# Performance work log

Hardware: AMD Instinct MI355X
Metric: run time of the kernel (lower is better)

Reference implementation:

```python
import jax, jax.numpy as jnp
import numpy as np

B, T, IN, H, OUT = 4096, 7, 512, 1024, 512


def setup_inputs() -> dict:
    key = jax.random.key(0)
    ks = jax.random.split(key, 13)
    s = 0.05  # weight init scale to keep gates/tanh unsaturated
    return {
        "x": jax.random.normal(ks[0], (B, T, IN), jnp.float32),
        "W_ih1": jax.random.normal(ks[1], (3 * H, IN), jnp.float32) * s,
        "W_hh1": jax.random.normal(ks[2], (3 * H, H), jnp.float32) * s,
        "b_ih1": jax.random.normal(ks[3], (3 * H,), jnp.float32) * s,
        "b_hh1": jax.random.normal(ks[4], (3 * H,), jnp.float32) * s,
        "W_ih2": jax.random.normal(ks[5], (3 * H, H), jnp.float32) * s,
        "W_hh2": jax.random.normal(ks[6], (3 * H, H), jnp.float32) * s,
        "b_ih2": jax.random.normal(ks[7], (3 * H,), jnp.float32) * s,
        "b_hh2": jax.random.normal(ks[8], (3 * H,), jnp.float32) * s,
        "Wo1": jax.random.normal(ks[9], (OUT, H), jnp.float32) * s,
        "bo1": jax.random.normal(ks[10], (OUT,), jnp.float32) * s,
        "Wo2": jax.random.normal(ks[11], (OUT, H), jnp.float32) * s,
        "bo2": jax.random.normal(ks[12], (OUT,), jnp.float32) * s,
    }


def gru_cell(x, h, W_ih, W_hh, b_ih, b_hh):
    # torch.nn.GRUCell math, gate order (r, z, n)
    gi = x @ W_ih.T + b_ih          # [B, 3H]
    gh = h @ W_hh.T + b_hh          # [B, 3H]
    i_r, i_z, i_n = jnp.split(gi, 3, axis=-1)
    h_r, h_z, h_n = jnp.split(gh, 3, axis=-1)
    r = jax.nn.sigmoid(i_r + h_r)
    z = jax.nn.sigmoid(i_z + h_z)
    n = jnp.tanh(i_n + r * h_n)
    return (1.0 - z) * n + z * h


def reference(x, W_ih1, W_hh1, b_ih1, b_hh1, W_ih2, W_hh2, b_ih2, b_hh2,
              Wo1, bo1, Wo2, bo2):
    batch = x.shape[0]
    h1_0 = jnp.zeros((batch, H), x.dtype)
    h2_0 = jnp.zeros((batch, H), x.dtype)

    def step(carry, x_t):
        h1, h2 = carry
        h1 = gru_cell(x_t, h1, W_ih1, W_hh1, b_ih1, b_hh1)
        h2 = gru_cell(h1, h2, W_ih2, W_hh2, b_ih2, b_hh2)
        out = jnp.tanh(h1 @ Wo1.T + bo1) + jnp.tanh(h2 @ Wo2.T + bo2)
        # s_t_cached starts as T zeros and only T steps run, so the popped
        # cached state is always zeros: mse(h2, 0) == mean(h2**2)
        aux = jnp.mean(jnp.square(h2))
        return (h1, h2), (out, aux)

    xs = jnp.swapaxes(x, 0, 1)  # [T, B, IN]
    _, (outs, auxs) = jax.lax.scan(step, (h1_0, h2_0), xs)
    outputs = jnp.swapaxes(outs, 0, 1)  # [B, T, OUT]
    aux_loss = jnp.sum(auxs)
    return outputs, aux_loss
```

## Files before the change

### kernel.cpp

```cpp
#include <hip/hip_runtime.h>
#include <cstdint>

#define BB   4096
#define TT   7
#define INF  512
#define HH   1024
#define OUTF 512
#define G3   3072

typedef short bf16x8 __attribute__((ext_vector_type(8)));
typedef float f32x4  __attribute__((ext_vector_type(4)));

static __device__ __forceinline__ unsigned short f2bf(float f) {
  unsigned u = __float_as_uint(f);
  unsigned r = ((u >> 16) & 1u) + 0x7FFFu;
  return (unsigned short)((u + r) >> 16);
}
static __device__ __forceinline__ float bf2f(unsigned short s) {
  return __uint_as_float(((unsigned)s) << 16);
}

#define GLDS16(gp, lp)                                                        \
  __builtin_amdgcn_global_load_lds(                                           \
      (const __attribute__((address_space(1))) void*)(gp),                    \
      (__attribute__((address_space(3))) void*)(lp), 16, 0, 0)

__device__ __forceinline__ int xcd_swz(int bid, int nwg) {
  return (bid & 7) * (nwg >> 3) + (bid >> 3);
}

__global__ __launch_bounds__(256)
void cvt_f32_to_bf16_x4(const float* __restrict__ in, unsigned short* __restrict__ out, int n4) {
  int i = blockIdx.x * 256 + threadIdx.x;
  if (i >= n4) return;
  const float4 v = ((const float4*)in)[i];
  ushort4 o;
  o.x = f2bf(v.x); o.y = f2bf(v.y); o.z = f2bf(v.z); o.w = f2bf(v.w);
  ((ushort4*)out)[i] = o;
}

template<int BM, int BN, int WM, int WN, int GN>
__device__ __forceinline__ void gemm_core(
    const unsigned short* __restrict__ A, long lda, long bm,
    const unsigned short* __restrict__ Wp, long ldw, int K,
    const float* __restrict__ biasp,
    void* __restrict__ Cp, long ldc,
    const float* __restrict__ addp, long ldadd, int mode)
{
  constexpr int AR = (BM * 8) / 256;
  constexpr int WR = (BN * 8) / 256;
  __shared__ __attribute__((aligned(16))) unsigned short sm[(BM + BN) * 64];
  unsigned short* As = sm;
  unsigned short* Ws = sm + BM * 64;
  __attribute__((address_space(3))) unsigned short* lAs =
      (__attribute__((address_space(3))) unsigned short*)As;
  __attribute__((address_space(3))) unsigned short* lWs =
      (__attribute__((address_space(3))) unsigned short*)Ws;

  const int tid  = threadIdx.x;
  const int lane = tid & 63;
  const int wid  = tid >> 6;
  const int wr = (wid / GN) * (WM * 16);
  const int wc = (wid % GN) * (WN * 16);
  const int fr = lane & 15;
  const int q2 = lane >> 4;

  const unsigned short* gpa[AR];
  const unsigned short* gpw[WR];
  int lofa[AR], lofw[WR];
#pragma unroll
  for (int r = 0; r < AR; ++r) {
    const int id = r * 256 + tid;
    const int row = id >> 3, cc = id & 7;
    gpa[r] = A + (bm + row) * lda + (cc ^ (row & 7)) * 8;
    lofa[r] = id * 8;
  }
#pragma unroll
  for (int r = 0; r < WR; ++r) {
    const int id = r * 256 + tid;
    const int row = id >> 3, cc = id & 7;
    gpw[r] = Wp + (long)row * ldw + (cc ^ (row & 7)) * 8;
    lofw[r] = id * 8;
  }

  f32x4 acc[WM][WN] = {};
  for (int kt = 0; kt < K; kt += 64) {
    if (kt) __syncthreads();
#pragma unroll
    for (int r = 0; r < AR; ++r) GLDS16(gpa[r] + kt, lAs + lofa[r]);
#pragma unroll
    for (int r = 0; r < WR; ++r) GLDS16(gpw[r] + kt, lWs + lofw[r]);
    __syncthreads();

#pragma unroll
    for (int ks = 0; ks < 2; ++ks) {
      bf16x8 af[WM], wf[WN];
#pragma unroll
      for (int i = 0; i < WM; ++i) {
        const int row = wr + i * 16 + fr;
        const int ch  = (ks * 4 + q2) ^ (row & 7);
        af[i] = *(const bf16x8*)&As[row * 64 + ch * 8];
      }
#pragma unroll
      for (int i = 0; i < WN; ++i) {
        const int row = wc + i * 16 + fr;
        const int ch  = (ks * 4 + q2) ^ (row & 7);
        wf[i] = *(const bf16x8*)&Ws[row * 64 + ch * 8];
      }
#pragma unroll
      for (int mi = 0; mi < WM; ++mi)
#pragma unroll
        for (int ni = 0; ni < WN; ++ni)
          acc[mi][ni] = __builtin_amdgcn_mfma_f32_16x16x32_bf16(af[mi], wf[ni], acc[mi][ni], 0, 0, 0);
    }
  }

  const int q = lane >> 4;
#pragma unroll
  for (int ni = 0; ni < WN; ++ni) {
    const int col = wc + ni * 16 + fr;
    const float bv = biasp[col];
#pragma unroll
    for (int mi = 0; mi < WM; ++mi) {
      const long row = bm + wr + mi * 16 + q * 4;
#pragma unroll
      for (int j = 0; j < 4; ++j) {
        const float v = acc[mi][ni][j] + bv;
        if (mode == 0)      ((float*)Cp)[(row + j) * ldc + col] = v;
        else if (mode == 1) ((float*)Cp)[(row + j) * ldc + col] = tanhf(v);
        else if (mode == 2) ((float*)Cp)[(row + j) * ldc + col] = tanhf(v) + addp[(row + j) * ldadd + col];
        else                ((unsigned short*)Cp)[(row + j) * ldc + col] = f2bf(v);
      }
    }
  }
}

__global__ __launch_bounds__(256)
void k_gi1(const unsigned short* __restrict__ A, long lda,
           const unsigned short* __restrict__ W, const float* __restrict__ bias,
           unsigned short* __restrict__ C, int gx)
{
  const int wg = xcd_swz(blockIdx.x, gridDim.x);
  const int bx = wg % gx, by = wg / gx;
  gemm_core<128,128,4,4,2>(A, lda, (long)bx * 128, W + (long)by * 128 * INF, INF, INF,
                           bias + by * 128, C + by * 128, G3, nullptr, 0, 3);
}

__global__ __launch_bounds__(256)
void k_gh_dual(const unsigned short* __restrict__ h1b, const unsigned short* __restrict__ h2b,
               const unsigned short* __restrict__ W1, const unsigned short* __restrict__ W2,
               const float* __restrict__ b1, const float* __restrict__ b2,
               float* __restrict__ gh1, float* __restrict__ gh2)
{
  const int wg = xcd_swz(blockIdx.x, gridDim.x);
  const int bx = wg % 32;
  const int by = (wg / 32) % 24;
  const int z  = wg / (32 * 24);
  const unsigned short* Aa = z ? h2b : h1b;
  const unsigned short* Ww = (z ? W2 : W1) + (long)by * 128 * HH;
  const float* bias = (z ? b2 : b1) + by * 128;
  float* C = (z ? gh2 : gh1) + by * 128;
  gemm_core<128,128,4,4,2>(Aa, HH, (long)bx * 128, Ww, HH, HH, bias, C, G3, nullptr, 0, 0);
}

__global__ __launch_bounds__(256)
void k_gi2_o1(const unsigned short* __restrict__ h1b,
              const unsigned short* __restrict__ Wih2, const float* __restrict__ bih2,
              float* __restrict__ gi2,
              const unsigned short* __restrict__ Wo1, const float* __restrict__ bo1,
              float* __restrict__ o1t)
{
  const int wg = xcd_swz(blockIdx.x, gridDim.x);
  const int bx = wg % 32;
  const int by = wg / 32;
  const bool g = (by < 24);
  const int bo = by - 24;
  const unsigned short* Ww = g ? (Wih2 + (long)by * 128 * HH) : (Wo1 + (long)bo * 128 * HH);
  const float* bias        = g ? (bih2 + by * 128)            : (bo1 + bo * 128);
  void* C                  = g ? (void*)(gi2 + by * 128)      : (void*)(o1t + bo * 128);
  const long ldc           = g ? (long)G3 : (long)OUTF;
  gemm_core<128,128,4,4,2>(h1b, HH, (long)bx * 128, Ww, HH, HH, bias, C, ldc,
                           nullptr, 0, g ? 0 : 1);
}

__global__ __launch_bounds__(256)
void k_o2_out(const unsigned short* __restrict__ h2b,
              const unsigned short* __restrict__ Wo2, const float* __restrict__ bo2,
              const float* __restrict__ o1t, float* __restrict__ outp)
{
  const int wg = xcd_swz(blockIdx.x, gridDim.x);
  const int bx = wg % 64;
  const int by = wg / 64;
  gemm_core<64,64,2,2,2>(h2b, HH, (long)bx * 64, Wo2 + (long)by * 64 * HH, HH, HH,
                         bo2 + by * 64, outp + by * 64, (long)TT * OUTF,
                         o1t + by * 64, OUTF, 2);
}

template<bool GIBF>
__global__ __launch_bounds__(256)
void k_gate(const void* __restrict__ gi, long gistride,
            const float* __restrict__ gh,
            unsigned short* __restrict__ hb,
            float* __restrict__ auxp)
{
  const int i4 = blockIdx.x * 256 + threadIdx.x;
  const int e  = i4 << 2;
  const int b = e >> 10;
  const int c = e & 1023;
  f32x4 ir, iz, inn;
  if (GIBF) {
    const unsigned short* g = (const unsigned short*)gi + (long)b * gistride + c;
    const ushort4 a0 = *(const ushort4*)(g);
    const ushort4 a1 = *(const ushort4*)(g + HH);
    const ushort4 a2 = *(const ushort4*)(g + 2 * HH);
    ir  = f32x4{bf2f(a0.x), bf2f(a0.y), bf2f(a0.z), bf2f(a0.w)};
    iz  = f32x4{bf2f(a1.x), bf2f(a1.y), bf2f(a1.z), bf2f(a1.w)};
    inn = f32x4{bf2f(a2.x), bf2f(a2.y), bf2f(a2.z), bf2f(a2.w)};
  } else {
    const float* g = (const float*)gi + (long)b * gistride + c;
    ir = *(const f32x4*)g; iz = *(const f32x4*)(g + HH); inn = *(const f32x4*)(g + 2 * HH);
  }
  const float* ghp = gh + (long)b * G3 + c;
  const f32x4 hr = *(const f32x4*)ghp;
  const f32x4 hz = *(const f32x4*)(ghp + HH);
  const f32x4 hn = *(const f32x4*)(ghp + 2 * HH);
  const ushort4 ho = *(const ushort4*)(hb + e);
  const f32x4 h = f32x4{bf2f(ho.x), bf2f(ho.y), bf2f(ho.z), bf2f(ho.w)};
  f32x4 hnew;
  float vsum = 0.f;
#pragma unroll
  for (int j = 0; j < 4; ++j) {
    const float r = 1.f / (1.f + __expf(-(ir[j] + hr[j])));
    const float z = 1.f / (1.f + __expf(-(iz[j] + hz[j])));
    const float n = tanhf(inn[j] + r * hn[j]);
    hnew[j] = (1.f - z) * n + z * h[j];
    vsum += hnew[j] * hnew[j];
  }
  ushort4 o;
  o.x = f2bf(hnew[0]); o.y = f2bf(hnew[1]); o.z = f2bf(hnew[2]); o.w = f2bf(hnew[3]);
  *(ushort4*)(hb + e) = o;
  if (auxp != nullptr) {
#pragma unroll
    for (int off = 32; off > 0; off >>= 1) vsum += __shfl_down(vsum, off);
    __shared__ float wsum[4];
    if ((threadIdx.x & 63) == 0) wsum[threadIdx.x >> 6] = vsum;
    __syncthreads();
    if (threadIdx.x == 0) auxp[blockIdx.x] = wsum[0] + wsum[1] + wsum[2] + wsum[3];
  }
}

__global__ __launch_bounds__(256)
void aux_reduce(const float* __restrict__ p, int n, float* __restrict__ out, float scale) {
  float s = 0.f;
  for (int i = threadIdx.x; i < n; i += 256) s += p[i];
#pragma unroll
  for (int off = 32; off > 0; off >>= 1) s += __shfl_down(s, off);
  __shared__ float wsum[4];
  if ((threadIdx.x & 63) == 0) wsum[threadIdx.x >> 6] = s;
  __syncthreads();
  if (threadIdx.x == 0) out[0] = (wsum[0] + wsum[1] + wsum[2] + wsum[3]) * scale;
}

extern "C" void kernel_launch(void* const* d_in, const int* in_sizes, int n_in,
                              void* d_out, int out_size, void* d_ws, size_t ws_size,
                              hipStream_t stream) {
  const float* x    = (const float*)d_in[0];
  const float* Wih1 = (const float*)d_in[1];
  const float* Whh1 = (const float*)d_in[2];
  const float* bih1 = (const float*)d_in[3];
  const float* bhh1 = (const float*)d_in[4];
  const float* Wih2 = (const float*)d_in[5];
  const float* Whh2 = (const float*)d_in[6];
  const float* bih2 = (const float*)d_in[7];
  const float* bhh2 = (const float*)d_in[8];
  const float* Wo1  = (const float*)d_in[9];
  const float* bo1  = (const float*)d_in[10];
  const float* Wo2  = (const float*)d_in[11];
  const float* bo2  = (const float*)d_in[12];

  char* ws = (char*)d_ws;
  size_t off = 0;
  auto alloc = [&](size_t bytes) {
    char* p = ws + off;
    off = (off + bytes + 255) & ~(size_t)255;
    return p;
  };

  unsigned short* xb    = (unsigned short*)alloc((size_t)BB * TT * INF * 2);
  unsigned short* wih1b = (unsigned short*)alloc((size_t)G3 * INF * 2);
  unsigned short* whh1b = (unsigned short*)alloc((size_t)G3 * HH * 2);
  unsigned short* wih2b = (unsigned short*)alloc((size_t)G3 * HH * 2);
  unsigned short* whh2b = (unsigned short*)alloc((size_t)G3 * HH * 2);
  unsigned short* wo1b  = (unsigned short*)alloc((size_t)OUTF * HH * 2);
  unsigned short* wo2b  = (unsigned short*)alloc((size_t)OUTF * HH * 2);
  unsigned short* h1b = (unsigned short*)alloc((size_t)BB * HH * 2);
  unsigned short* h2b = (unsigned short*)alloc((size_t)BB * HH * 2);
  float* gh1  = (float*)alloc((size_t)BB * G3 * 4);
  float* gh2  = (float*)alloc((size_t)BB * G3 * 4);
  float* o1t  = (float*)alloc((size_t)BB * OUTF * 4);
  float* auxp = (float*)alloc((size_t)TT * (BB * HH / 1024) * 4);
  float* gi2  = gh1;

  const size_t gi1_big   = (size_t)BB * TT * G3 * 2;
  const size_t gi1_small = (size_t)BB * G3 * 2;
  const bool hoist = (off + gi1_big + (size_t)(32 << 20)) <= ws_size;
  unsigned short* gi1b = (unsigned short*)alloc(hoist ? gi1_big : gi1_small);

  float* aux = (float*)d_out + (size_t)BB * TT * OUTF;

  auto cvt = [&](const float* src, unsigned short* dst, size_t n) {
    int n4 = (int)(n / 4);
    cvt_f32_to_bf16_x4<<<dim3((n4 + 255) / 256), dim3(256), 0, stream>>>(src, dst, n4);
  };
  cvt(x,    xb,    (size_t)BB * TT * INF);
  cvt(Wih1, wih1b, (size_t)G3 * INF);
  cvt(Whh1, whh1b, (size_t)G3 * HH);
  cvt(Wih2, wih2b, (size_t)G3 * HH);
  cvt(Whh2, whh2b, (size_t)G3 * HH);
  cvt(Wo1,  wo1b,  (size_t)OUTF * HH);
  cvt(Wo2,  wo2b,  (size_t)OUTF * HH);

  hipMemsetAsync(h1b, 0, (size_t)BB * HH * 2, stream);
  hipMemsetAsync(h2b, 0, (size_t)BB * HH * 2, stream);

  const dim3 blk(256);
  const int gateGrid = BB * HH / 1024;

  if (hoist)
    k_gi1<<<dim3(224 * 24), blk, 0, stream>>>(xb, INF, wih1b, bih1, gi1b, 224);

  for (int t = 0; t < TT; ++t) {
    if (!hoist)
      k_gi1<<<dim3(32 * 24), blk, 0, stream>>>(xb + (size_t)t * INF, (long)TT * INF,
                                               wih1b, bih1, gi1b, 32);
    k_gh_dual<<<dim3(32 * 24 * 2), blk, 0, stream>>>(h1b, h2b, whh1b, whh2b, bhh1, bhh2, gh1, gh2);
    k_gate<true><<<dim3(gateGrid), blk, 0, stream>>>(
        hoist ? gi1b + (size_t)t * G3 : gi1b, hoist ? (long)TT * G3 : (long)G3,
        gh1, h1b, nullptr);
    k_gi2_o1<<<dim3(32 * 28), blk, 0, stream>>>(h1b, wih2b, bih2, gi2, wo1b, bo1, o1t);
    k_gate<false><<<dim3(gateGrid), blk, 0, stream>>>(gi2, (long)G3, gh2, h2b,
                                                      auxp + (size_t)t * gateGrid);
    k_o2_out<<<dim3(64 * 8), blk, 0, stream>>>(h2b, wo2b, bo2, o1t,
                                               (float*)d_out + (size_t)t * OUTF);
  }
  aux_reduce<<<dim3(1), blk, 0, stream>>>(auxp, TT * gateGrid, aux,
                                          1.f / ((float)BB * (float)HH));
}
```

Baseline: 1.419 ms.

## Double-buffer GEMM LDS tiles and store gate pre-activations as bf16

The shared GEMM core now uses two LDS buffers. The next K tile's global-to-LDS loads are issued before the MFMAs on the current tile, which leaves one barrier per iteration and overlaps memory with compute. Separately, the gh1/gh2/gi2 gate pre-activation buffers are written and read as bf16 instead of fp32, roughly halving the traffic between the GEMMs and the gate kernels. The cost is double the LDS footprint per block, which may reduce occupancy, plus extra rounding error in the hidden-state gate inputs.

```diff
diff --git a/kernel.cpp b/kernel.cpp
--- a/kernel.cpp
+++ b/kernel.cpp
@@ -47,11 +47,13 @@
     void* __restrict__ Cp, long ldc,
     const float* __restrict__ addp, long ldadd, int mode)
 {
+  constexpr int ABUF = BM * 64;
+  constexpr int WBUF = BN * 64;
   constexpr int AR = (BM * 8) / 256;
   constexpr int WR = (BN * 8) / 256;
-  __shared__ __attribute__((aligned(16))) unsigned short sm[(BM + BN) * 64];
+  __shared__ __attribute__((aligned(16))) unsigned short sm[2 * (ABUF + WBUF)];
   unsigned short* As = sm;
-  unsigned short* Ws = sm + BM * 64;
+  unsigned short* Ws = sm + 2 * ABUF;
   __attribute__((address_space(3))) unsigned short* lAs =
       (__attribute__((address_space(3))) unsigned short*)As;
   __attribute__((address_space(3))) unsigned short* lWs =
@@ -83,14 +85,20 @@
     lofw[r] = id * 8;
   }
 
+#define STAGE(buf, kt) do {                                                   \
+    _Pragma("unroll")                                                         \
+    for (int r = 0; r < AR; ++r) GLDS16(gpa[r] + (kt), lAs + (buf) * ABUF + lofa[r]); \
+    _Pragma("unroll")                                                         \
+    for (int r = 0; r < WR; ++r) GLDS16(gpw[r] + (kt), lWs + (buf) * WBUF + lofw[r]); \
+  } while (0)
+
   f32x4 acc[WM][WN] = {};
-  for (int kt = 0; kt < K; kt += 64) {
-    if (kt) __syncthreads();
-#pragma unroll
-    for (int r = 0; r < AR; ++r) GLDS16(gpa[r] + kt, lAs + lofa[r]);
-#pragma unroll
-    for (int r = 0; r < WR; ++r) GLDS16(gpw[r] + kt, lWs + lofw[r]);
-    __syncthreads();
+  STAGE(0, 0);
+  __syncthreads();
+  const int NK = K >> 6;
+  for (int it = 0; it < NK; ++it) {
+    const int cur = it & 1;
+    if (it + 1 < NK) STAGE(cur ^ 1, (it + 1) << 6);
 
 #pragma unroll
     for (int ks = 0; ks < 2; ++ks) {
@@ -99,13 +107,13 @@
       for (int i = 0; i < WM; ++i) {
         const int row = wr + i * 16 + fr;
         const int ch  = (ks * 4 + q2) ^ (row & 7);
-        af[i] = *(const bf16x8*)&As[row * 64 + ch * 8];
+        af[i] = *(const bf16x8*)&As[cur * ABUF + row * 64 + ch * 8];
       }
 #pragma unroll
       for (int i = 0; i < WN; ++i) {
         const int row = wc + i * 16 + fr;
         const int ch  = (ks * 4 + q2) ^ (row & 7);
-        wf[i] = *(const bf16x8*)&Ws[row * 64 + ch * 8];
+        wf[i] = *(const bf16x8*)&Ws[cur * WBUF + row * 64 + ch * 8];
       }
 #pragma unroll
       for (int mi = 0; mi < WM; ++mi)
@@ -113,7 +121,9 @@
         for (int ni = 0; ni < WN; ++ni)
           acc[mi][ni] = __builtin_amdgcn_mfma_f32_16x16x32_bf16(af[mi], wf[ni], acc[mi][ni], 0, 0, 0);
     }
-  }
+    __syncthreads();
+  }
+#undef STAGE
 
   const int q = lane >> 4;
 #pragma unroll
@@ -150,7 +160,7 @@
 void k_gh_dual(const unsigned short* __restrict__ h1b, const unsigned short* __restrict__ h2b,
                const unsigned short* __restrict__ W1, const unsigned short* __restrict__ W2,
                const float* __restrict__ b1, const float* __restrict__ b2,
-               float* __restrict__ gh1, float* __restrict__ gh2)
+               unsigned short* __restrict__ gh1, unsigned short* __restrict__ gh2)
 {
   const int wg = xcd_swz(blockIdx.x, gridDim.x);
   const int bx = wg % 32;
@@ -159,14 +169,14 @@
   const unsigned short* Aa = z ? h2b : h1b;
   const unsigned short* Ww = (z ? W2 : W1) + (long)by * 128 * HH;
   const float* bias = (z ? b2 : b1) + by * 128;
-  float* C = (z ? gh2 : gh1) + by * 128;
-  gemm_core<128,128,4,4,2>(Aa, HH, (long)bx * 128, Ww, HH, HH, bias, C, G3, nullptr, 0, 0);
+  unsigned short* C = (z ? gh2 : gh1) + by * 128;
+  gemm_core<128,128,4,4,2>(Aa, HH, (long)bx * 128, Ww, HH, HH, bias, C, G3, nullptr, 0, 3);
 }
 
 __global__ __launch_bounds__(256)
 void k_gi2_o1(const unsigned short* __restrict__ h1b,
               const unsigned short* __restrict__ Wih2, const float* __restrict__ bih2,
-              float* __restrict__ gi2,
+              unsigned short* __restrict__ gi2,
               const unsigned short* __restrict__ Wo1, const float* __restrict__ bo1,
               float* __restrict__ o1t)
 {
@@ -180,7 +190,7 @@
   void* C                  = g ? (void*)(gi2 + by * 128)      : (void*)(o1t + bo * 128);
   const long ldc           = g ? (long)G3 : (long)OUTF;
   gemm_core<128,128,4,4,2>(h1b, HH, (long)bx * 128, Ww, HH, HH, bias, C, ldc,
-                           nullptr, 0, g ? 0 : 1);
+                           nullptr, 0, g ? 3 : 1);
 }
 
 __global__ __launch_bounds__(256)
@@ -196,10 +206,9 @@
                          o1t + by * 64, OUTF, 2);
 }
 
-template<bool GIBF>
-__global__ __launch_bounds__(256)
-void k_gate(const void* __restrict__ gi, long gistride,
-            const float* __restrict__ gh,
+__global__ __launch_bounds__(256)
+void k_gate(const unsigned short* __restrict__ gi, long gistride,
+            const unsigned short* __restrict__ gh,
             unsigned short* __restrict__ hb,
             float* __restrict__ auxp)
 {
@@ -207,23 +216,20 @@
   const int e  = i4 << 2;
   const int b = e >> 10;
   const int c = e & 1023;
-  f32x4 ir, iz, inn;
-  if (GIBF) {
-    const unsigned short* g = (const unsigned short*)gi + (long)b * gistride + c;
-    const ushort4 a0 = *(const ushort4*)(g);
-    const ushort4 a1 = *(const ushort4*)(g + HH);
-    const ushort4 a2 = *(const ushort4*)(g + 2 * HH);
-    ir  = f32x4{bf2f(a0.x), bf2f(a0.y), bf2f(a0.z), bf2f(a0.w)};
-    iz  = f32x4{bf2f(a1.x), bf2f(a1.y), bf2f(a1.z), bf2f(a1.w)};
-    inn = f32x4{bf2f(a2.x), bf2f(a2.y), bf2f(a2.z), bf2f(a2.w)};
-  } else {
-    const float* g = (const float*)gi + (long)b * gistride + c;
-    ir = *(const f32x4*)g; iz = *(const f32x4*)(g + HH); inn = *(const f32x4*)(g + 2 * HH);
-  }
-  const float* ghp = gh + (long)b * G3 + c;
-  const f32x4 hr = *(const f32x4*)ghp;
-  const f32x4 hz = *(const f32x4*)(ghp + HH);
-  const f32x4 hn = *(const f32x4*)(ghp + 2 * HH);
+  const unsigned short* g = gi + (long)b * gistride + c;
+  const ushort4 a0 = *(const ushort4*)(g);
+  const ushort4 a1 = *(const ushort4*)(g + HH);
+  const ushort4 a2 = *(const ushort4*)(g + 2 * HH);
+  const unsigned short* gg = gh + (long)b * G3 + c;
+  const ushort4 b0 = *(const ushort4*)(gg);
+  const ushort4 b1 = *(const ushort4*)(gg + HH);
+  const ushort4 b2 = *(const ushort4*)(gg + 2 * HH);
+  const f32x4 ir  = f32x4{bf2f(a0.x), bf2f(a0.y), bf2f(a0.z), bf2f(a0.w)};
+  const f32x4 iz  = f32x4{bf2f(a1.x), bf2f(a1.y), bf2f(a1.z), bf2f(a1.w)};
+  const f32x4 inn = f32x4{bf2f(a2.x), bf2f(a2.y), bf2f(a2.z), bf2f(a2.w)};
+  const f32x4 hr  = f32x4{bf2f(b0.x), bf2f(b0.y), bf2f(b0.z), bf2f(b0.w)};
+  const f32x4 hz  = f32x4{bf2f(b1.x), bf2f(b1.y), bf2f(b1.z), bf2f(b1.w)};
+  const f32x4 hn  = f32x4{bf2f(b2.x), bf2f(b2.y), bf2f(b2.z), bf2f(b2.w)};
   const ushort4 ho = *(const ushort4*)(hb + e);
   const f32x4 h = f32x4{bf2f(ho.x), bf2f(ho.y), bf2f(ho.z), bf2f(ho.w)};
   f32x4 hnew;
@@ -295,11 +301,11 @@
   unsigned short* wo2b  = (unsigned short*)alloc((size_t)OUTF * HH * 2);
   unsigned short* h1b = (unsigned short*)alloc((size_t)BB * HH * 2);
   unsigned short* h2b = (unsigned short*)alloc((size_t)BB * HH * 2);
-  float* gh1  = (float*)alloc((size_t)BB * G3 * 4);
-  float* gh2  = (float*)alloc((size_t)BB * G3 * 4);
+  unsigned short* gh1 = (unsigned short*)alloc((size_t)BB * G3 * 2);
+  unsigned short* gh2 = (unsigned short*)alloc((size_t)BB * G3 * 2);
   float* o1t  = (float*)alloc((size_t)BB * OUTF * 4);
   float* auxp = (float*)alloc((size_t)TT * (BB * HH / 1024) * 4);
-  float* gi2  = gh1;
+  unsigned short* gi2 = gh1;
 
   const size_t gi1_big   = (size_t)BB * TT * G3 * 2;
   const size_t gi1_small = (size_t)BB * G3 * 2;
@@ -334,12 +340,12 @@
       k_gi1<<<dim3(32 * 24), blk, 0, stream>>>(xb + (size_t)t * INF, (long)TT * INF,
                                                wih1b, bih1, gi1b, 32);
     k_gh_dual<<<dim3(32 * 24 * 2), blk, 0, stream>>>(h1b, h2b, whh1b, whh2b, bhh1, bhh2, gh1, gh2);
-    k_gate<true><<<dim3(gateGrid), blk, 0, stream>>>(
+    k_gate<<<dim3(gateGrid), blk, 0, stream>>>(
         hoist ? gi1b + (size_t)t * G3 : gi1b, hoist ? (long)TT * G3 : (long)G3,
         gh1, h1b, nullptr);
     k_gi2_o1<<<dim3(32 * 28), blk, 0, stream>>>(h1b, wih2b, bih2, gi2, wo1b, bo1, o1t);
-    k_gate<false><<<dim3(gateGrid), blk, 0, stream>>>(gi2, (long)G3, gh2, h2b,
-                                                      auxp + (size_t)t * gateGrid);
+    k_gate<<<dim3(gateGrid), blk, 0, stream>>>(gi2, (long)G3, gh2, h2b,
+                                               auxp + (size_t)t * gateGrid);
     k_o2_out<<<dim3(64 * 8), blk, 0, stream>>>(h2b, wo2b, bo2, o1t,
                                                (float*)d_out + (size_t)t * OUTF);
   }
```

After: 1.416 ms. Within noise of the previous version (-0.2%).
